# Optimization experiments

Measured on AMD Instinct MI355X. Metric: run time of the kernel, lower is better.

The kernel has to match this reference:

```python
import jax, jax.numpy as jnp
import numpy as np

B = 8192
IN = 512          # inputs feature dim (input_size[2])
CTX = 256         # context_input_size
CENTER = 512      # center_size
MIN_ = IN + CTX   # module_input_size = 768
FF = 1024         # n_ff_pre_units
RNN = 1024        # n_rnn_units
OUT = 512         # output_size
O2C = 256         # output_to_center_size
TOT = OUT + O2C   # total_output_size = 768


def setup_inputs() -> dict:
    key = jax.random.key(0)
    ks = jax.random.split(key, 12)
    return {
        "inputs": jax.random.normal(ks[0], (B, 1, IN), jnp.float32),
        "center_state": jax.random.normal(ks[1], (B, 1, CENTER), jnp.float32),
        "module_state": jax.random.normal(ks[2], (B, 1, RNN), jnp.float32),
        # reading_weights: truncated normal stddev 0.1 in TF; plain normal*0.1 is fine for a math reference
        "W_read": jax.random.normal(ks[3], (CENTER, CTX), jnp.float32) * 0.1,
        "W_pre": jax.random.normal(ks[4], (MIN_, FF), jnp.float32) * (1.0 / np.sqrt(MIN_)),
        "b_pre": jnp.zeros((FF,), jnp.float32),
        "Wx": jax.random.normal(ks[5], (FF, RNN), jnp.float32) * (1.0 / np.sqrt(FF)),
        "Wh": jax.random.normal(ks[6], (RNN, RNN), jnp.float32) * (1.0 / np.sqrt(RNN)),
        "b_rnn": jnp.zeros((RNN,), jnp.float32),
        "W_post": jax.random.normal(ks[7], (RNN, TOT), jnp.float32) * (1.0 / np.sqrt(RNN)),
        "b_post": jnp.zeros((TOT,), jnp.float32),
    }


def reference(inputs, center_state, module_state, W_read, W_pre, b_pre, Wx, Wh, b_rnn, W_post, b_post):
    # tf.clip_by_norm(W, 1.0): global Frobenius norm clip
    norm = jnp.sqrt(jnp.sum(W_read * W_read))
    W_clip = W_read * (1.0 / jnp.maximum(norm, 1.0))
    # context read: [B,1,CENTER] @ [CENTER,CTX] -> [B,1,CTX]
    context = jnp.einsum("btc,cd->btd", center_state, W_clip)
    module_inputs = jnp.concatenate([inputs, context], axis=2)  # [B,1,MIN_]
    rnn_in = jax.nn.relu(jnp.einsum("btf,fg->btg", module_inputs, W_pre) + b_pre)
    # SimpleRNNCell: h' = tanh(x Wx + h Wh + b)
    h_new = jnp.tanh(jnp.einsum("btf,fg->btg", rnn_in, Wx)
                     + jnp.einsum("btf,fg->btg", module_state, Wh) + b_rnn)
    module_output = jax.nn.relu(jnp.einsum("btf,fg->btg", h_new, W_post) + b_post)
    network_output = module_output[:, :, :OUT]
    module_output_to_center = module_output[:, :, OUT:]
    return (network_output, module_output_to_center, h_new)
```

## Files before the change

### kernel.cpp

```cpp
#include <hip/hip_runtime.h>

typedef __bf16 bf16x8 __attribute__((ext_vector_type(8)));
typedef float  f32x4  __attribute__((ext_vector_type(4)));
typedef unsigned short ushort8 __attribute__((ext_vector_type(8)));

#define B_ROWS 8192
#define OUT_D  512
#define O2C_D  256
#define TOT_D  768
#define MIN_D  768
#define RNN_D  1024

__device__ __forceinline__ unsigned short f2bf(float f) {
    unsigned int u = __builtin_bit_cast(unsigned int, f);
    u = (u + 0x7fff + ((u >> 16) & 1)) >> 16;
    return (unsigned short)u;
}

__device__ __forceinline__ void load_lds16(const void* g, void* l) {
    __builtin_amdgcn_global_load_lds(
        (const __attribute__((address_space(1))) unsigned int*)g,
        (__attribute__((address_space(3))) unsigned int*)l, 16, 0, 0);
}

__launch_bounds__(256)
__global__ void prep_all(const float* __restrict__ Wread, float* __restrict__ partials,
                         const float* __restrict__ Wpre, const float* __restrict__ Wx,
                         const float* __restrict__ Wh,  const float* __restrict__ Wpost,
                         unsigned short* __restrict__ WpreT, unsigned short* __restrict__ WxhT,
                         unsigned short* __restrict__ WpostT, unsigned short* __restrict__ WreadT,
                         const float* __restrict__ center, const float* __restrict__ inputs,
                         const float* __restrict__ mstate,
                         unsigned short* __restrict__ csB, unsigned short* __restrict__ miB,
                         unsigned short* __restrict__ rnB) {
    const int bid = blockIdx.x;
    const int tid = threadIdx.x;
    if (bid < 128) {
        __shared__ float red[4];
        const float* p = Wread + bid * 1024 + tid * 4;
        f32x4 v = *(const f32x4*)p;
        float s = v[0]*v[0] + v[1]*v[1] + v[2]*v[2] + v[3]*v[3];
        #pragma unroll
        for (int off = 32; off > 0; off >>= 1) s += __shfl_down(s, off, 64);
        if ((tid & 63) == 0) red[tid >> 6] = s;
        __syncthreads();
        if (tid == 0) partials[bid] = red[0] + red[1] + red[2] + red[3];
        return;
    }
    if (bid < 1984) {
        int g = (bid - 128) * 256 + tid;
        const float* W; unsigned short* out; int N, ostride;
        if (g < 98304)        { W = Wpre;  out = WpreT;        N = 1024; ostride = 768;  }
        else if (g < 229376)  { g -= 98304;  W = Wx;    out = WxhT;        N = 1024; ostride = 2048; }
        else if (g < 360448)  { g -= 229376; W = Wh;    out = WxhT + 1024; N = 1024; ostride = 2048; }
        else if (g < 458752)  { g -= 360448; W = Wpost; out = WpostT;      N = 768;  ostride = 1024; }
        else                  { g -= 458752; W = Wread; out = WreadT;      N = 256;  ostride = 512;  }
        int n  = g % N;
        int kg = g / N;
        ushort8 o;
        #pragma unroll
        for (int j = 0; j < 8; ++j)
            o[j] = f2bf(W[(long)(kg * 8 + j) * N + n]);
        *(ushort8*)(out + (long)n * ostride + kg * 8) = o;
        return;
    }
    long g = (long)(bid - 1984) * 256 + tid;
    const float* src; unsigned short* dst; int logc, ostride;
    if (g < 524288)       { src = center; dst = csB;        logc = 9;  ostride = 512;  }
    else if (g < 1048576) { g -= 524288;  src = inputs; dst = miB;        logc = 9;  ostride = 768;  }
    else                  { g -= 1048576; src = mstate; dst = rnB + 1024; logc = 10; ostride = 2048; }
    long e = g * 8;
    long row = e >> logc;
    int  col = (int)(e & ((1 << logc) - 1));
    f32x4 v0 = *(const f32x4*)(src + e);
    f32x4 v1 = *(const f32x4*)(src + e + 4);
    ushort8 o;
    o[0] = f2bf(v0[0]); o[1] = f2bf(v0[1]); o[2] = f2bf(v0[2]); o[3] = f2bf(v0[3]);
    o[4] = f2bf(v1[0]); o[5] = f2bf(v1[1]); o[6] = f2bf(v1[2]); o[7] = f2bf(v1[3]);
    *(ushort8*)(dst + row * (long)ostride + col) = o;
}

template<int MODE, int BNT>
__launch_bounds__(256, 4)
__global__ void gemm_bt(const unsigned short* __restrict__ A,
                        const unsigned short* __restrict__ Bt,
                        int K, const float* __restrict__ bias,
                        unsigned short* __restrict__ outB, int ldob,
                        float* __restrict__ outF, int ldof) {
    constexpr int U   = BNT / 32;
    constexpr int BJ  = BNT / 32;
    __shared__ alignas(16) unsigned short smem[128 * 64 + BNT * 64];
    unsigned short* sA = smem;
    unsigned short* sB = smem + 128 * 64;

    const int tid  = threadIdx.x;
    const int wave = tid >> 6;
    const int lane = tid & 63;
    const int bm = blockIdx.x, bn = blockIdx.y;
    const int wm = wave & 1, wn = wave >> 1;
    const int lr = lane >> 4;
    const int lc = lane & 15;
    const int sw = lc & 7;

    f32x4 acc[4][U] = {};

    long aoff[4], boff[BJ];
    #pragma unroll
    for (int j = 0; j < 4; ++j) {
        const int c   = tid + j * 256;
        const int row = c >> 3;
        const int kg  = (c & 7) ^ (row & 7);
        aoff[j] = (long)(bm * 128 + row) * K + kg * 8;
    }
    #pragma unroll
    for (int j = 0; j < BJ; ++j) {
        const int c   = tid + j * 256;
        const int row = c >> 3;
        const int kg  = (c & 7) ^ (row & 7);
        boff[j] = (long)(bn * BNT + row) * K + kg * 8;
    }

    for (int k0 = 0; k0 < K; k0 += 64) {
        #pragma unroll
        for (int j = 0; j < 4; ++j)
            load_lds16(A + aoff[j] + k0, (char*)sA + j * 4096 + wave * 1024);
        #pragma unroll
        for (int j = 0; j < BJ; ++j)
            load_lds16(Bt + boff[j] + k0, (char*)sB + j * 4096 + wave * 1024);
        __syncthreads();

        #pragma unroll
        for (int kh = 0; kh < 2; ++kh) {
            const int ch = (kh * 4 + lr) ^ sw;
            bf16x8 af[4], bfr[U];
            #pragma unroll
            for (int t = 0; t < 4; ++t)
                af[t] = *(const bf16x8*)(sA + (wm * 64 + t * 16 + lc) * 64 + ch * 8);
            #pragma unroll
            for (int u = 0; u < U; ++u)
                bfr[u] = *(const bf16x8*)(sB + (wn * (BNT / 2) + u * 16 + lc) * 64 + ch * 8);
            #pragma unroll
            for (int i = 0; i < 4; ++i)
                #pragma unroll
                for (int u = 0; u < U; ++u)
                    acc[i][u] = __builtin_amdgcn_mfma_f32_16x16x32_bf16(af[i], bfr[u], acc[i][u], 0, 0, 0);
        }
        __syncthreads();
    }

    float sc = 1.f;
    if constexpr (MODE == 0) {
        float s = 0.f;
        for (int i = 0; i < 128; ++i) s += bias[i];
        sc = 1.f / fmaxf(sqrtf(s), 1.f);
    }
    #pragma unroll
    for (int u = 0; u < U; ++u) {
        float bv = 0.f;
        if constexpr (MODE != 0) bv = bias[bn * BNT + wn * (BNT / 2) + u * 16 + lc];
        #pragma unroll
        for (int tm = 0; tm < 4; ++tm)
            #pragma unroll
            for (int r = 0; r < 4; ++r) {
                float v = acc[tm][u][r];
                if constexpr (MODE == 0) v *= sc;
                else v += bv;
                if constexpr (MODE == 1 || MODE == 3) v = fmaxf(v, 0.f);
                acc[tm][u][r] = v;
            }
    }

    const int ctcol = wn * (BNT / 2);

    if constexpr (MODE <= 2) {
        unsigned short* Cb = smem;
        #pragma unroll
        for (int u = 0; u < U; ++u)
            #pragma unroll
            for (int tm = 0; tm < 4; ++tm)
                #pragma unroll
                for (int r = 0; r < 4; ++r)
                    Cb[(wm * 64 + tm * 16 + lr * 4 + r) * BNT + ctcol + u * 16 + lc] =
                        f2bf(acc[tm][u][r]);
        __syncthreads();
        constexpr int RC = BNT / 8;
        constexpr int CPT = 128 * RC / 256;
        #pragma unroll
        for (int t = 0; t < CPT; ++t) {
            const int chunk = t * 256 + tid;
            const int row = chunk / RC;
            const int c8  = chunk % RC;
            ushort8 val = *(ushort8*)(Cb + row * BNT + c8 * 8);
            *(ushort8*)(outB + (long)(bm * 128 + row) * ldob + bn * BNT + c8 * 8) = val;
        }
    }

    if constexpr (MODE == 3) {
        float* Cf = (float*)smem;
        #pragma unroll
        for (int h = 0; h < 2; ++h) {
            __syncthreads();
            if (wm == h) {
                #pragma unroll
                for (int u = 0; u < U; ++u)
                    #pragma unroll
                    for (int tm = 0; tm < 4; ++tm)
                        #pragma unroll
                        for (int r = 0; r < 4; ++r)
                            Cf[(tm * 16 + lr * 4 + r) * BNT + ctcol + u * 16 + lc] =
                                acc[tm][u][r];
            }
            __syncthreads();
            constexpr int RCF = BNT / 4;
            constexpr int CPTF = 64 * RCF / 256;
            #pragma unroll
            for (int t = 0; t < CPTF; ++t) {
                const int chunk = t * 256 + tid;
                const int row = chunk / RCF;
                const int c4  = chunk % RCF;
                f32x4 val = *(f32x4*)(Cf + row * BNT + c4 * 4);
                const long grow = bm * 128 + h * 64 + row;
                if (bn * BNT < OUT_D)
                    *(f32x4*)(outF + grow * OUT_D + bn * BNT + c4 * 4) = val;
                else
                    *(f32x4*)(outF + (long)B_ROWS * OUT_D + grow * O2C_D
                              + (bn * BNT - OUT_D) + c4 * 4) = val;
            }
        }
    }
}

template<int MODE>
__launch_bounds__(512, 1)
__global__ void gemm256(const unsigned short* __restrict__ A,
                        const unsigned short* __restrict__ Bt,
                        int K, const float* __restrict__ bias,
                        unsigned short* __restrict__ outB, int ldob,
                        float* __restrict__ outF, int ldof) {
    constexpr int ABUF = 256 * 64;
    constexpr int BBUF = 128 * 64;
    constexpr int BUFE = ABUF + BBUF;
    __shared__ alignas(16) unsigned short smem[3 * BUFE];

    const int tid  = threadIdx.x;
    const int wave = tid >> 6;
    const int lane = tid & 63;
    const int i  = blockIdx.x;
    const int bm = (i & 7) + 8 * ((i >> 3) & 3);
    const int bn = i >> 5;
    const int wm = wave >> 1, wn = wave & 1;
    const int lr = lane >> 4;
    const int lc = lane & 15;
    const int sw = lc & 7;
    const int nt = K >> 6;

    f32x4 acc[4][4] = {};

    long aoff[4], boff[2];
    #pragma unroll
    for (int j = 0; j < 4; ++j) {
        const int c   = tid + j * 512;
        const int row = c >> 3;
        const int kg  = (c & 7) ^ (row & 7);
        aoff[j] = (long)(bm * 256 + row) * K + kg * 8;
    }
    #pragma unroll
    for (int j = 0; j < 2; ++j) {
        const int c   = tid + j * 512;
        const int row = c >> 3;
        const int kg  = (c & 7) ^ (row & 7);
        boff[j] = (long)(bn * 128 + row) * K + kg * 8;
    }

    auto stageA2 = [&](int buf, int k0, int jlo) {
        char* base = (char*)(smem + buf * BUFE);
        load_lds16(A + aoff[jlo]     + k0, base + jlo       * 8192 + wave * 1024);
        load_lds16(A + aoff[jlo + 1] + k0, base + (jlo + 1) * 8192 + wave * 1024);
    };
    auto stageB1 = [&](int buf, int k0, int j) {
        char* base = (char*)(smem + buf * BUFE) + ABUF * 2;
        load_lds16(Bt + boff[j] + k0, base + j * 8192 + wave * 1024);
    };
    auto dsA = [&](int buf, int kh, bf16x8* af) {
        const unsigned short* sA = smem + buf * BUFE;
        const int ch = (kh * 4 + lr) ^ sw;
        #pragma unroll
        for (int m = 0; m < 4; ++m)
            af[m] = *(const bf16x8*)(sA + (wm * 64 + m * 16 + lc) * 64 + ch * 8);
    };
    auto dsB = [&](int buf, int kh, bf16x8* bf) {
        const unsigned short* sB = smem + buf * BUFE + ABUF;
        const int ch = (kh * 4 + lr) ^ sw;
        #pragma unroll
        for (int n = 0; n < 4; ++n)
            bf[n] = *(const bf16x8*)(sB + (wn * 64 + n * 16 + lc) * 64 + ch * 8);
    };

    stageA2(0, 0, 0); stageA2(0, 0, 2); stageB1(0, 0, 0); stageB1(0, 0, 1);
    if (nt > 1) {
        stageA2(1, 64, 0); stageA2(1, 64, 2); stageB1(1, 64, 0); stageB1(1, 64, 1);
        asm volatile("s_waitcnt vmcnt(6)" ::: "memory");
    } else {
        asm volatile("s_waitcnt vmcnt(0)" ::: "memory");
    }
    __builtin_amdgcn_s_barrier();

    int cur = 0;
    for (int t = 0; t < nt; ++t) {
        const int  k2   = (t + 2) << 6;
        const bool st   = (t + 2) < nt;
        const int  nbuf = (cur >= 1) ? cur - 1 : cur + 2;

        bf16x8 af[4], bf[4];

        if (st) { stageA2(nbuf, k2, 0); stageB1(nbuf, k2, 0); }
        dsA(cur, 0, af); dsB(cur, 0, bf);
        __builtin_amdgcn_s_barrier();
        asm volatile("s_waitcnt lgkmcnt(0)" ::: "memory");
        __builtin_amdgcn_sched_barrier(0);
        __builtin_amdgcn_s_setprio(1);
        #pragma unroll
        for (int m = 0; m < 4; ++m)
            #pragma unroll
            for (int n = 0; n < 4; ++n)
                acc[m][n] = __builtin_amdgcn_mfma_f32_16x16x32_bf16(af[m], bf[n], acc[m][n], 0, 0, 0);
        __builtin_amdgcn_s_setprio(0);
        __builtin_amdgcn_s_barrier();

        if (st) { stageA2(nbuf, k2, 2); stageB1(nbuf, k2, 1); }
        dsA(cur, 1, af); dsB(cur, 1, bf);
        if (t + 1 < nt) {
            if (st) asm volatile("s_waitcnt vmcnt(6)" ::: "memory");
            else    asm volatile("s_waitcnt vmcnt(0)" ::: "memory");
        }
        __builtin_amdgcn_s_barrier();
        asm volatile("s_waitcnt lgkmcnt(0)" ::: "memory");
        __builtin_amdgcn_sched_barrier(0);
        __builtin_amdgcn_s_setprio(1);
        #pragma unroll
        for (int m = 0; m < 4; ++m)
            #pragma unroll
            for (int n = 0; n < 4; ++n)
                acc[m][n] = __builtin_amdgcn_mfma_f32_16x16x32_bf16(af[m], bf[n], acc[m][n], 0, 0, 0);
        __builtin_amdgcn_s_setprio(0);
        __builtin_amdgcn_s_barrier();

        cur = (cur == 2) ? 0 : cur + 1;
    }

    #pragma unroll
    for (int n = 0; n < 4; ++n) {
        const float bv = bias[bn * 128 + wn * 64 + n * 16 + lc];
        #pragma unroll
        for (int m = 0; m < 4; ++m)
            #pragma unroll
            for (int r = 0; r < 4; ++r) {
                float v = acc[m][n][r] + bv;
                if constexpr (MODE == 2) v = tanhf(v);
                else                     v = fmaxf(v, 0.f);
                acc[m][n][r] = v;
            }
    }

    if constexpr (MODE <= 2) {
        unsigned short* Cb = smem;
        __syncthreads();
        #pragma unroll
        for (int m = 0; m < 4; ++m)
            #pragma unroll
            for (int n = 0; n < 4; ++n)
                #pragma unroll
                for (int r = 0; r < 4; ++r)
                    Cb[(wm * 64 + m * 16 + lr * 4 + r) * 128 + wn * 64 + n * 16 + lc] =
                        f2bf(acc[m][n][r]);
        __syncthreads();
        #pragma unroll
        for (int tch = 0; tch < 8; ++tch) {
            const int chunk = tch * 512 + tid;
            const int row = chunk >> 4;
            const int c8  = chunk & 15;
            ushort8 v = *(ushort8*)(Cb + row * 128 + c8 * 8);
            *(ushort8*)(outB + (long)(bm * 256 + row) * ldob + bn * 128 + c8 * 8) = v;
        }
    }

    if constexpr (MODE >= 2) {
        float* Cf = (float*)smem;
        __syncthreads();
        #pragma unroll
        for (int m = 0; m < 4; ++m)
            #pragma unroll
            for (int n = 0; n < 4; ++n)
                #pragma unroll
                for (int r = 0; r < 4; ++r)
                    Cf[(wm * 64 + m * 16 + lr * 4 + r) * 128 + wn * 64 + n * 16 + lc] =
                        acc[m][n][r];
        __syncthreads();
        #pragma unroll
        for (int tch = 0; tch < 16; ++tch) {
            const int chunk = tch * 512 + tid;
            const int row = chunk >> 5;
            const int c4  = chunk & 31;
            f32x4 v = *(f32x4*)(Cf + row * 128 + c4 * 4);
            const long grow = bm * 256 + row;
            if constexpr (MODE == 2) {
                *(f32x4*)(outF + grow * ldof + bn * 128 + c4 * 4) = v;
            } else {
                if (bn < 4)
                    *(f32x4*)(outF + grow * OUT_D + bn * 128 + c4 * 4) = v;
                else
                    *(f32x4*)(outF + (long)B_ROWS * OUT_D + grow * O2C_D
                              + (bn - 4) * 128 + c4 * 4) = v;
            }
        }
    }
}

extern "C" void kernel_launch(void* const* d_in, const int* in_sizes, int n_in,
                              void* d_out, int out_size, void* d_ws, size_t ws_size,
                              hipStream_t stream) {
    const float* inputs = (const float*)d_in[0];
    const float* center = (const float*)d_in[1];
    const float* mstate = (const float*)d_in[2];
    const float* W_read = (const float*)d_in[3];
    const float* W_pre  = (const float*)d_in[4];
    const float* b_pre  = (const float*)d_in[5];
    const float* Wx     = (const float*)d_in[6];
    const float* Wh     = (const float*)d_in[7];
    const float* b_rnn  = (const float*)d_in[8];
    const float* W_post = (const float*)d_in[9];
    const float* b_post = (const float*)d_in[10];
    float* out = (float*)d_out;

    char* ws = (char*)d_ws;
    float* partials = (float*)ws;
    unsigned short* WreadT = (unsigned short*)(ws + 1024);
    unsigned short* WpreT  = WreadT + 256 * 512;
    unsigned short* WxhT   = WpreT  + 1024 * 768;
    unsigned short* WpostT = WxhT   + (long)1024 * 2048;
    unsigned short* csB    = WpostT + 768 * 1024;
    unsigned short* miB    = csB + (long)B_ROWS * 512;
    unsigned short* rnB    = miB + (long)B_ROWS * MIN_D;
    unsigned short* hB     = rnB + (long)B_ROWS * 2048;

    prep_all<<<10176, 256, 0, stream>>>(W_read, partials,
                                        W_pre, Wx, Wh, W_post,
                                        WpreT, WxhT, WpostT, WreadT,
                                        center, inputs, mstate, csB, miB, rnB);

    gemm_bt<0, 64><<<dim3(64, 4), 256, 0, stream>>>(csB, WreadT, 512, partials,
                                                    miB + 512, MIN_D, nullptr, 0);
    gemm256<1><<<256, 512, 0, stream>>>(miB, WpreT, 768, b_pre,
                                        rnB, 2048, nullptr, 0);
    gemm256<2><<<256, 512, 0, stream>>>(rnB, WxhT, 2048, b_rnn,
                                        hB, RNN_D, out + (long)B_ROWS * TOT_D, RNN_D);
    gemm256<3><<<192, 512, 0, stream>>>(hB, WpostT, 1024, b_post,
                                        nullptr, 0, out, 0);
}
```

Before: 244.9 us.

## Merge half-tile GEMM phases into one stage per K tile with single barrier

Restructures the triple-buffered GEMM main loop so that each 64-wide K tile issues all six global-to-LDS loads at once, reads both K halves of fragments from LDS, then runs 32 MFMAs back to back. This cuts four barriers per iteration down to one, reducing synchronisation overhead and lengthening the uninterrupted MFMA run. In exchange it doubles the fragment registers held at once, which may raise register pressure, and it loses the finer interleaving of loads with compute.

```diff
diff --git a/kernel.cpp b/kernel.cpp
--- a/kernel.cpp
+++ b/kernel.cpp
@@ -272,14 +272,15 @@
         boff[j] = (long)(bn * 128 + row) * K + kg * 8;
     }
 
-    auto stageA2 = [&](int buf, int k0, int jlo) {
+    auto stage6 = [&](int buf, int k0) {
         char* base = (char*)(smem + buf * BUFE);
-        load_lds16(A + aoff[jlo]     + k0, base + jlo       * 8192 + wave * 1024);
-        load_lds16(A + aoff[jlo + 1] + k0, base + (jlo + 1) * 8192 + wave * 1024);
-    };
-    auto stageB1 = [&](int buf, int k0, int j) {
-        char* base = (char*)(smem + buf * BUFE) + ABUF * 2;
-        load_lds16(Bt + boff[j] + k0, base + j * 8192 + wave * 1024);
+        #pragma unroll
+        for (int j = 0; j < 4; ++j)
+            load_lds16(A + aoff[j] + k0, base + j * 8192 + wave * 1024);
+        char* bbase = base + ABUF * 2;
+        #pragma unroll
+        for (int j = 0; j < 2; ++j)
+            load_lds16(Bt + boff[j] + k0, bbase + j * 8192 + wave * 1024);
     };
     auto dsA = [&](int buf, int kh, bf16x8* af) {
         const unsigned short* sA = smem + buf * BUFE;
@@ -296,9 +297,9 @@
             bf[n] = *(const bf16x8*)(sB + (wn * 64 + n * 16 + lc) * 64 + ch * 8);
     };
 
-    stageA2(0, 0, 0); stageA2(0, 0, 2); stageB1(0, 0, 0); stageB1(0, 0, 1);
+    stage6(0, 0);
     if (nt > 1) {
-        stageA2(1, 64, 0); stageA2(1, 64, 2); stageB1(1, 64, 0); stageB1(1, 64, 1);
+        stage6(1, 64);
         asm volatile("s_waitcnt vmcnt(6)" ::: "memory");
     } else {
         asm volatile("s_waitcnt vmcnt(0)" ::: "memory");
@@ -307,15 +308,14 @@
 
     int cur = 0;
     for (int t = 0; t < nt; ++t) {
-        const int  k2   = (t + 2) << 6;
         const bool st   = (t + 2) < nt;
         const int  nbuf = (cur >= 1) ? cur - 1 : cur + 2;
 
-        bf16x8 af[4], bf[4];
-
-        if (st) { stageA2(nbuf, k2, 0); stageB1(nbuf, k2, 0); }
-        dsA(cur, 0, af); dsB(cur, 0, bf);
-        __builtin_amdgcn_s_barrier();
+        if (st) stage6(nbuf, (t + 2) << 6);
+
+        bf16x8 af0[4], bf0[4], af1[4], bf1[4];
+        dsA(cur, 0, af0); dsB(cur, 0, bf0);
+        dsA(cur, 1, af1); dsB(cur, 1, bf1);
         asm volatile("s_waitcnt lgkmcnt(0)" ::: "memory");
         __builtin_amdgcn_sched_barrier(0);
         __builtin_amdgcn_s_setprio(1);
@@ -323,26 +323,18 @@
         for (int m = 0; m < 4; ++m)
             #pragma unroll
             for (int n = 0; n < 4; ++n)
-                acc[m][n] = __builtin_amdgcn_mfma_f32_16x16x32_bf16(af[m], bf[n], acc[m][n], 0, 0, 0);
+                acc[m][n] = __builtin_amdgcn_mfma_f32_16x16x32_bf16(af0[m], bf0[n], acc[m][n], 0, 0, 0);
+        #pragma unroll
+        for (int m = 0; m < 4; ++m)
+            #pragma unroll
+            for (int n = 0; n < 4; ++n)
+                acc[m][n] = __builtin_amdgcn_mfma_f32_16x16x32_bf16(af1[m], bf1[n], acc[m][n], 0, 0, 0);
         __builtin_amdgcn_s_setprio(0);
-        __builtin_amdgcn_s_barrier();
-
-        if (st) { stageA2(nbuf, k2, 2); stageB1(nbuf, k2, 1); }
-        dsA(cur, 1, af); dsB(cur, 1, bf);
+
         if (t + 1 < nt) {
             if (st) asm volatile("s_waitcnt vmcnt(6)" ::: "memory");
             else    asm volatile("s_waitcnt vmcnt(0)" ::: "memory");
         }
-        __builtin_amdgcn_s_barrier();
-        asm volatile("s_waitcnt lgkmcnt(0)" ::: "memory");
-        __builtin_amdgcn_sched_barrier(0);
-        __builtin_amdgcn_s_setprio(1);
-        #pragma unroll
-        for (int m = 0; m < 4; ++m)
-            #pragma unroll
-            for (int n = 0; n < 4; ++n)
-                acc[m][n] = __builtin_amdgcn_mfma_f32_16x16x32_bf16(af[m], bf[n], acc[m][n], 0, 0, 0);
-        __builtin_amdgcn_s_setprio(0);
         __builtin_amdgcn_s_barrier();
 
         cur = (cur == 2) ? 0 : cur + 1;
```

After: 237.6 us. -3.0%, faster.
